# Kernel optimization log

Hardware: AMD Instinct MI355X
Metric: run time of the kernel (lower is better)

The kernel has to match this reference:

```python
import jax, jax.numpy as jnp
import numpy as np

E = 8          # number of tasks/experts (grown via new_task in the original)
B = 4096       # batch
CH, HT, WD = 3, 32, 32
D = CH * HT * WD   # 3072 flattened image dim
H = 1024       # hidden_dim
L = 512        # latent_dim
C = 100        # classes
TEMP = 2.0     # self.temperature


def setup_inputs() -> dict:
    key = jax.random.key(0)
    ks = jax.random.split(key, 32)
    def w(k, shape, fan_in):
        return jax.random.normal(k, shape, jnp.float32) * (1.0 / np.sqrt(fan_in))
    z = lambda shape: jnp.zeros(shape, jnp.float32)
    return {
        "x": jax.random.normal(ks[0], (B, CH, HT, WD), jnp.float32),
        # Gate autoencoder (per-expert stacked): encoder D->H->H->L, decoder L->H->H->D
        "enc_w0": w(ks[1], (E, D, H), D), "enc_b0": z((E, H)),
        "enc_w1": w(ks[2], (E, H, H), H), "enc_b1": z((E, H)),
        "enc_w2": w(ks[3], (E, H, L), H), "enc_b2": z((E, L)),
        "dec_w0": w(ks[4], (E, L, H), L), "dec_b0": z((E, H)),
        "dec_w1": w(ks[5], (E, H, H), H), "dec_b1": z((E, H)),
        "dec_w2": w(ks[6], (E, H, D), H), "dec_b2": z((E, D)),
        # Expert MLP (per-expert stacked): L->H->H->C
        "exp_w0": w(ks[7], (E, L, H), L), "exp_b0": z((E, H)),
        "exp_w1": w(ks[8], (E, H, H), H), "exp_b1": z((E, H)),
        "exp_w2": w(ks[9], (E, H, C), H), "exp_b2": z((E, C)),
    }


def reference(x, enc_w0, enc_b0, enc_w1, enc_b1, enc_w2, enc_b2,
              dec_w0, dec_b0, dec_w1, dec_b1, dec_w2, dec_b2,
              exp_w0, exp_b0, exp_w1, exp_b1, exp_w2, exp_b2):
    relu = jax.nn.relu
    b = x.shape[0]
    xf = x.reshape(b, -1)                                            # [B, D]
    # --- all gates in one batched pass (replaces python loop over gates) ---
    h = relu(jnp.einsum('bd,edh->ebh', xf, enc_w0) + enc_b0[:, None, :])
    h = relu(jnp.einsum('ebh,ehk->ebk', h, enc_w1) + enc_b1[:, None, :])
    lat = jnp.einsum('ebh,ehl->ebl', h, enc_w2) + enc_b2[:, None, :]  # [E, B, L]
    g = relu(jnp.einsum('ebl,elh->ebh', lat, dec_w0) + dec_b0[:, None, :])
    g = relu(jnp.einsum('ebh,ehk->ebk', g, dec_w1) + dec_b1[:, None, :])
    recon_flat = jnp.einsum('ebh,ehd->ebd', g, dec_w2) + dec_b2[:, None, :]  # [E, B, D]
    # L1 reconstruction error, mean over (C,H,W) == mean over flattened D
    err = jnp.mean(jnp.abs(recon_flat - xf[None]), axis=-1)          # [E, B]
    relevance_scores = jax.nn.softmax(-err / TEMP, axis=0)           # softmax over experts
    indices = jnp.argmin(err, axis=0)                                # [B]
    min_err = jnp.min(err, axis=0)                                   # [B]
    mask = jnp.arange(err.shape[0])[:, None] == indices[None, :]     # [E, B] bool
    # --- all experts densely, then select per-sample winner (same math as
    # the original masked gather/MLP/scatter: each row gets its argmin expert) ---
    e = relu(jnp.einsum('ebl,elh->ebh', lat, exp_w0) + exp_b0[:, None, :])
    e = relu(jnp.einsum('ebh,ehk->ebk', e, exp_w1) + exp_b1[:, None, :])
    exp_out = jnp.einsum('ebh,ehc->ebc', e, exp_w2) + exp_b2[:, None, :]  # [E, B, C]
    logits = jnp.take_along_axis(exp_out, indices[None, :, None], axis=0)[0]  # [B, C]
    reconstructions = recon_flat.reshape((err.shape[0],) + x.shape)  # [E, B, C, H, W]
    return (logits, reconstructions, indices, min_err, relevance_scores, mask)
```

## Files before the change

kernel.cpp:

```cpp
#include <hip/hip_runtime.h>
#include <hip/hip_fp16.h>

#define E_ 8
#define B_ 4096
#define D_ 3072
#define H_ 1024
#define L_ 512
#define C_ 100

#define RECON_OFF  409600ull
#define IDX_OFF    101072896ull
#define MINERR_OFF 101076992ull
#define REL_OFF    101081088ull
#define MASK_OFF   101113856ull

typedef _Float16 half8 __attribute__((ext_vector_type(8)));
typedef float floatx4 __attribute__((ext_vector_type(4)));

#define AS1 __attribute__((address_space(1)))
#define AS3 __attribute__((address_space(3)))

__device__ __forceinline__ void gl16(const void* g, void* l) {
  __builtin_amdgcn_global_load_lds((const AS1 unsigned int*)g, (AS3 unsigned int*)l, 16, 0, 0);
}

enum { OM_HILO = 0, OM_HI = 1, OM_F32 = 2, OM_RECON = 3 };

template <int OM, bool RELU, bool SPLIT>
__launch_bounds__(256, 2)
__global__ void gemm_k(const _Float16* __restrict__ Ah, const _Float16* __restrict__ Al,
                       const _Float16* __restrict__ Bh, const _Float16* __restrict__ Bl,
                       const float* __restrict__ bias, int biasN,
                       _Float16* __restrict__ Oh, _Float16* __restrict__ Ol,
                       float* __restrict__ Of, const float* __restrict__ Xf,
                       float* __restrict__ errOut,
                       int N, int K, int Npad, int Nstore, long aStrideE)
{
  const int M = B_;
  const int mBlocks = M >> 7;
  const int bx = blockIdx.x;
  const int mb = bx % mBlocks;
  const int nb = bx / mBlocks;
  const int e = blockIdx.y;
  const int m0 = mb << 7, n0 = nb << 7;
  const int tid = threadIdx.x;
  const int wave = tid >> 6, lane = tid & 63;
  const int wy = wave >> 1, wx = wave & 1;
  const int q = lane >> 4, t = lane & 15;

  __shared__ __align__(16) _Float16 sAh[128 * 32];
  __shared__ __align__(16) _Float16 sBh[128 * 32];
  __shared__ __align__(16) _Float16 sAl[SPLIT ? 128 * 32 : 8];
  __shared__ __align__(16) _Float16 sBl[SPLIT ? 128 * 32 : 8];
  __shared__ float ebuf[OM == OM_RECON ? 256 : 1];

  const size_t aoff = (size_t)(m0 + wave * 32 + (lane >> 2)) * K + (lane & 3) * 8;
  const size_t boff = (size_t)(n0 + wave * 32 + (lane >> 2)) * K + (lane & 3) * 8;
  const _Float16* pAh = Ah + (size_t)e * aStrideE + aoff;
  const _Float16* pBh = Bh + (size_t)e * Npad * K + boff;
  const _Float16* pAl = SPLIT ? (Al + (size_t)e * aStrideE + aoff) : (const _Float16*)nullptr;
  const _Float16* pBl = SPLIT ? (Bl + (size_t)e * Npad * K + boff) : (const _Float16*)nullptr;
  _Float16* dAh = &sAh[(wave * 32) * 32];
  _Float16* dBh = &sBh[(wave * 32) * 32];
  _Float16* dAl = &sAl[SPLIT ? (wave * 32) * 32 : 0];
  _Float16* dBl = &sBl[SPLIT ? (wave * 32) * 32 : 0];

  floatx4 acc[4][4] = {};
  floatx4 acx[4][4] = {};

  for (int kt = 0; kt < K; kt += 32) {
    __syncthreads();
    gl16(pAh, dAh);
    gl16(pAh + (size_t)16 * K, dAh + 16 * 32);
    gl16(pBh, dBh);
    gl16(pBh + (size_t)16 * K, dBh + 16 * 32);
    if (SPLIT) {
      gl16(pAl, dAl);
      gl16(pAl + (size_t)16 * K, dAl + 16 * 32);
      gl16(pBl, dBl);
      gl16(pBl + (size_t)16 * K, dBl + 16 * 32);
    }
    pAh += 32; pBh += 32;
    if (SPLIT) { pAl += 32; pBl += 32; }
    __syncthreads();

    half8 a_h[4], b_h[4], a_l[4], b_l[4];
#pragma unroll
    for (int i = 0; i < 4; ++i) {
      a_h[i] = *(const half8*)&sAh[(wy * 64 + i * 16 + t) * 32 + q * 8];
      b_h[i] = *(const half8*)&sBh[(wx * 64 + i * 16 + t) * 32 + q * 8];
      if (SPLIT) {
        a_l[i] = *(const half8*)&sAl[(wy * 64 + i * 16 + t) * 32 + q * 8];
        b_l[i] = *(const half8*)&sBl[(wx * 64 + i * 16 + t) * 32 + q * 8];
      }
    }
#pragma unroll
    for (int i = 0; i < 4; ++i)
#pragma unroll
      for (int j = 0; j < 4; ++j) {
        acc[i][j] = __builtin_amdgcn_mfma_f32_16x16x32_f16(a_h[i], b_h[j], acc[i][j], 0, 0, 0);
        if (SPLIT) {
          acx[i][j] = __builtin_amdgcn_mfma_f32_16x16x32_f16(a_h[i], b_l[j], acx[i][j], 0, 0, 0);
          acx[i][j] = __builtin_amdgcn_mfma_f32_16x16x32_f16(a_l[i], b_h[j], acx[i][j], 0, 0, 0);
        }
      }
  }

  float esum[4][4];
#pragma unroll
  for (int i = 0; i < 4; ++i)
#pragma unroll
    for (int r = 0; r < 4; ++r) esum[i][r] = 0.0f;

#pragma unroll
  for (int j = 0; j < 4; ++j) {
    const int gcol = n0 + wx * 64 + j * 16 + t;
    float bj = 0.0f;
    if (OM == OM_F32) { if (gcol < biasN) bj = bias[e * biasN + gcol]; }
    else bj = bias[e * biasN + gcol];
#pragma unroll
    for (int i = 0; i < 4; ++i)
#pragma unroll
      for (int r = 0; r < 4; ++r) {
        float v = acc[i][j][r];
        if (SPLIT) v += acx[i][j][r] * (1.0f / 4096.0f);
        v += bj;
        if (RELU) v = fmaxf(v, 0.0f);
        const int grow = m0 + wy * 64 + i * 16 + q * 4 + r;
        if (OM == OM_HILO) {
          const size_t o = (size_t)e * M * N + (size_t)grow * N + gcol;
          _Float16 h = (_Float16)v;
          Oh[o] = h;
          Ol[o] = (_Float16)((v - (float)h) * 4096.0f);
        } else if (OM == OM_HI) {
          Oh[(size_t)e * M * N + (size_t)grow * N + gcol] = (_Float16)v;
        } else if (OM == OM_F32) {
          if (gcol < Nstore)
            Of[(size_t)e * M * Nstore + (size_t)grow * Nstore + gcol] = v;
        } else {
          const size_t o = (size_t)e * M * N + (size_t)grow * N + gcol;
          Of[o] = v;
          esum[i][r] += fabsf(v - Xf[(size_t)grow * N + gcol]);
        }
      }
  }

  if (OM == OM_RECON) {
#pragma unroll
    for (int i = 0; i < 4; ++i)
#pragma unroll
      for (int r = 0; r < 4; ++r) {
        float s = esum[i][r];
        s += __shfl_xor(s, 1, 16);
        s += __shfl_xor(s, 2, 16);
        s += __shfl_xor(s, 4, 16);
        s += __shfl_xor(s, 8, 16);
        if (t == 0) ebuf[(wy * 64 + i * 16 + q * 4 + r) * 2 + wx] = s;
      }
    __syncthreads();
    if (tid < 128)
      atomicAdd(&errOut[(size_t)e * M + m0 + tid], ebuf[tid * 2] + ebuf[tid * 2 + 1]);
  }
}

__global__ void xsplit_k(const float* __restrict__ x, _Float16* __restrict__ xh,
                         _Float16* __restrict__ xl, int n)
{
  int i = blockIdx.x * 256 + threadIdx.x;
  if (i < n) {
    float v = x[i];
    _Float16 h = (_Float16)v;
    xh[i] = h;
    xl[i] = (_Float16)((v - (float)h) * 4096.0f);
  }
}

__global__ void wprep_k(const float* __restrict__ W, _Float16* __restrict__ Th,
                        _Float16* __restrict__ Tl, int K, int N, int Npad)
{
  __shared__ float tile[32][33];
  const int e = blockIdx.z;
  const int k0 = blockIdx.x * 32, n0 = blockIdx.y * 32;
  const int tx = threadIdx.x, ty = threadIdx.y;
  const float* We = W + (size_t)e * K * N;
#pragma unroll
  for (int s = 0; s < 4; ++s) {
    int k = k0 + ty + s * 8, n = n0 + tx;
    tile[ty + s * 8][tx] = (n < N) ? We[(size_t)k * N + n] : 0.0f;
  }
  __syncthreads();
#pragma unroll
  for (int s = 0; s < 4; ++s) {
    int n = n0 + ty + s * 8, k = k0 + tx;
    float v = tile[tx][ty + s * 8];
    size_t o = ((size_t)e * Npad + n) * K + k;
    _Float16 h = (_Float16)v;
    Th[o] = h;
    if (Tl) Tl[o] = (_Float16)((v - (float)h) * 4096.0f);
  }
}

__global__ void finalize_k(const float* __restrict__ err, float* __restrict__ out,
                           int* __restrict__ idxbuf)
{
  int b = blockIdx.x * 256 + threadIdx.x;
  if (b >= B_) return;
  float ev[E_];
  float mn = 3.4e38f;
  int am = 0;
#pragma unroll
  for (int e = 0; e < E_; ++e) {
    float v = err[(size_t)e * B_ + b] * (1.0f / 3072.0f);
    ev[e] = v;
    if (v < mn) { mn = v; am = e; }
  }
  float den = 0.0f, w[E_];
#pragma unroll
  for (int e = 0; e < E_; ++e) { w[e] = expf((mn - ev[e]) * 0.5f); den += w[e]; }
  float inv = 1.0f / den;
  out[IDX_OFF + b] = (float)am;
  out[MINERR_OFF + b] = mn;
#pragma unroll
  for (int e = 0; e < E_; ++e) {
    out[REL_OFF + (size_t)e * B_ + b] = w[e] * inv;
    out[MASK_OFF + (size_t)e * B_ + b] = (e == am) ? 1.0f : 0.0f;
  }
  idxbuf[b] = am;
}

__global__ void gather_k(const float* __restrict__ expout, const int* __restrict__ idx,
                         float* __restrict__ out)
{
  int b = blockIdx.x;
  int c = threadIdx.x;
  if (c < C_) out[(size_t)b * C_ + c] = expout[((size_t)idx[b] * B_ + b) * C_ + c];
}

extern "C" void kernel_launch(void* const* d_in, const int* in_sizes, int n_in,
                              void* d_out, int out_size, void* d_ws, size_t ws_size,
                              hipStream_t stream)
{
  const float* x      = (const float*)d_in[0];
  const float* enc_w0 = (const float*)d_in[1];
  const float* enc_b0 = (const float*)d_in[2];
  const float* enc_w1 = (const float*)d_in[3];
  const float* enc_b1 = (const float*)d_in[4];
  const float* enc_w2 = (const float*)d_in[5];
  const float* enc_b2 = (const float*)d_in[6];
  const float* dec_w0 = (const float*)d_in[7];
  const float* dec_b0 = (const float*)d_in[8];
  const float* dec_w1 = (const float*)d_in[9];
  const float* dec_b1 = (const float*)d_in[10];
  const float* dec_w2 = (const float*)d_in[11];
  const float* dec_b2 = (const float*)d_in[12];
  const float* exp_w0 = (const float*)d_in[13];
  const float* exp_b0 = (const float*)d_in[14];
  const float* exp_w1 = (const float*)d_in[15];
  const float* exp_b1 = (const float*)d_in[16];
  const float* exp_w2 = (const float*)d_in[17];
  const float* exp_b2 = (const float*)d_in[18];

  char* ws = (char*)d_ws;
  _Float16* xh     = (_Float16*)(ws + 0);
  _Float16* xl     = (_Float16*)(ws + 25165824);
  _Float16* WTh    = (_Float16*)(ws + 50331648);
  _Float16* WTl    = (_Float16*)(ws + 100663296);
  _Float16* lath   = (_Float16*)(ws + 150994944);
  _Float16* latl   = (_Float16*)(ws + 184549376);
  _Float16* g2h    = (_Float16*)(ws + 218103808);
  _Float16* g2l    = (_Float16*)(ws + 285212672);
  float*    expout = (float*)   (ws + 352321536);
  float*    errb   = (float*)   (ws + 365428736);
  int*      idxb   = (int*)     (ws + 365559808);

  float* out = (float*)d_out;
  float* recon = out + RECON_OFF;
  _Float16* bufAh = (_Float16*)recon;
  _Float16* bufAl = bufAh + (size_t)E_ * B_ * H_;
  _Float16* bufBh = bufAl + (size_t)E_ * B_ * H_;
  _Float16* bufBl = bufBh + (size_t)E_ * B_ * H_;

  hipMemsetAsync(errb, 0, (size_t)E_ * B_ * 4, stream);
  xsplit_k<<<(B_ * D_ + 255) / 256, 256, 0, stream>>>(x, xh, xl, B_ * D_);

  dim3 wb(32, 8);

  wprep_k<<<dim3(96, 32, E_), wb, 0, stream>>>(enc_w0, WTh, WTl, 3072, 1024, 1024);
  gemm_k<OM_HILO, true, true><<<dim3(32 * 8, E_), 256, 0, stream>>>(
      xh, xl, WTh, WTl, enc_b0, 1024, bufAh, bufAl, nullptr, nullptr, nullptr,
      1024, 3072, 1024, 1024, 0L);
  wprep_k<<<dim3(32, 32, E_), wb, 0, stream>>>(enc_w1, WTh, WTl, 1024, 1024, 1024);
  gemm_k<OM_HILO, true, true><<<dim3(32 * 8, E_), 256, 0, stream>>>(
      bufAh, bufAl, WTh, WTl, enc_b1, 1024, bufBh, bufBl, nullptr, nullptr, nullptr,
      1024, 1024, 1024, 1024, (long)B_ * H_);
  wprep_k<<<dim3(32, 16, E_), wb, 0, stream>>>(enc_w2, WTh, WTl, 1024, 512, 512);
  gemm_k<OM_HILO, false, true><<<dim3(32 * 4, E_), 256, 0, stream>>>(
      bufBh, bufBl, WTh, WTl, enc_b2, 512, lath, latl, nullptr, nullptr, nullptr,
      512, 1024, 512, 512, (long)B_ * H_);
  wprep_k<<<dim3(16, 32, E_), wb, 0, stream>>>(exp_w0, WTh, nullptr, 512, 1024, 1024);
  gemm_k<OM_HI, true, false><<<dim3(32 * 8, E_), 256, 0, stream>>>(
      lath, nullptr, WTh, nullptr, exp_b0, 1024, bufAh, nullptr, nullptr, nullptr, nullptr,
      1024, 512, 1024, 1024, (long)B_ * L_);
  wprep_k<<<dim3(32, 32, E_), wb, 0, stream>>>(exp_w1, WTh, nullptr, 1024, 1024, 1024);
  gemm_k<OM_HI, true, false><<<dim3(32 * 8, E_), 256, 0, stream>>>(
      bufAh, nullptr, WTh, nullptr, exp_b1, 1024, bufBh, nullptr, nullptr, nullptr, nullptr,
      1024, 1024, 1024, 1024, (long)B_ * H_);
  wprep_k<<<dim3(32, 4, E_), wb, 0, stream>>>(exp_w2, WTh, nullptr, 1024, 100, 128);
  gemm_k<OM_F32, false, false><<<dim3(32 * 1, E_), 256, 0, stream>>>(
      bufBh, nullptr, WTh, nullptr, exp_b2, 100, nullptr, nullptr, expout, nullptr, nullptr,
      128, 1024, 128, 100, (long)B_ * H_);
  wprep_k<<<dim3(16, 32, E_), wb, 0, stream>>>(dec_w0, WTh, WTl, 512, 1024, 1024);
  gemm_k<OM_HILO, true, true><<<dim3(32 * 8, E_), 256, 0, stream>>>(
      lath, latl, WTh, WTl, dec_b0, 1024, bufAh, bufAl, nullptr, nullptr, nullptr,
      1024, 512, 1024, 1024, (long)B_ * L_);
  wprep_k<<<dim3(32, 32, E_), wb, 0, stream>>>(dec_w1, WTh, WTl, 1024, 1024, 1024);
  gemm_k<OM_HILO, true, true><<<dim3(32 * 8, E_), 256, 0, stream>>>(
      bufAh, bufAl, WTh, WTl, dec_b1, 1024, g2h, g2l, nullptr, nullptr, nullptr,
      1024, 1024, 1024, 1024, (long)B_ * H_);
  wprep_k<<<dim3(32, 96, E_), wb, 0, stream>>>(dec_w2, WTh, WTl, 1024, 3072, 3072);
  gemm_k<OM_RECON, false, true><<<dim3(32 * 24, E_), 256, 0, stream>>>(
      g2h, g2l, WTh, WTl, dec_b2, 3072, nullptr, nullptr, recon, x, errb,
      3072, 1024, 3072, 3072, (long)B_ * H_);

  finalize_k<<<(B_ + 255) / 256, 256, 0, stream>>>(errb, out, idxb);
  gather_k<<<B_, 128, 0, stream>>>(expout, idxb, out);
}
```

Measured before the change: 2.969 ms.

## Merge split-precision accumulators, swizzle LDS layout, raise occupancy bounds

Removes the scaling of low-part fp16 residuals so the cross-term MFMAs accumulate into the main accumulator, eliminating a second 4x4 accumulator array and cutting register pressure. Launch bounds are raised so more blocks can reside per CU. An XOR swizzle is applied to the LDS tile columns at load and read time to reduce bank conflicts. Unscaled residuals risk fp16 subnormal precision loss in the split-precision products.

```diff
diff --git a/kernel.cpp b/kernel.cpp
--- a/kernel.cpp
+++ b/kernel.cpp
@@ -27,7 +27,7 @@
 enum { OM_HILO = 0, OM_HI = 1, OM_F32 = 2, OM_RECON = 3 };
 
 template <int OM, bool RELU, bool SPLIT>
-__launch_bounds__(256, 2)
+__launch_bounds__(256, SPLIT ? 3 : 4)
 __global__ void gemm_k(const _Float16* __restrict__ Ah, const _Float16* __restrict__ Al,
                        const _Float16* __restrict__ Bh, const _Float16* __restrict__ Bl,
                        const float* __restrict__ bias, int biasN,
@@ -54,8 +54,9 @@
   __shared__ __align__(16) _Float16 sBl[SPLIT ? 128 * 32 : 8];
   __shared__ float ebuf[OM == OM_RECON ? 256 : 1];
 
-  const size_t aoff = (size_t)(m0 + wave * 32 + (lane >> 2)) * K + (lane & 3) * 8;
-  const size_t boff = (size_t)(n0 + wave * 32 + (lane >> 2)) * K + (lane & 3) * 8;
+  const int swzc = ((lane & 3) ^ ((lane >> 3) & 3)) * 8;
+  const size_t aoff = (size_t)(m0 + wave * 32 + (lane >> 2)) * K + swzc;
+  const size_t boff = (size_t)(n0 + wave * 32 + (lane >> 2)) * K + swzc;
   const _Float16* pAh = Ah + (size_t)e * aStrideE + aoff;
   const _Float16* pBh = Bh + (size_t)e * Npad * K + boff;
   const _Float16* pAl = SPLIT ? (Al + (size_t)e * aStrideE + aoff) : (const _Float16*)nullptr;
@@ -65,8 +66,9 @@
   _Float16* dAl = &sAl[SPLIT ? (wave * 32) * 32 : 0];
   _Float16* dBl = &sBl[SPLIT ? (wave * 32) * 32 : 0];
 
+  const int rcol = (q ^ ((t >> 1) & 3)) * 8;
+
   floatx4 acc[4][4] = {};
-  floatx4 acx[4][4] = {};
 
   for (int kt = 0; kt < K; kt += 32) {
     __syncthreads();
@@ -87,11 +89,11 @@
     half8 a_h[4], b_h[4], a_l[4], b_l[4];
 #pragma unroll
     for (int i = 0; i < 4; ++i) {
-      a_h[i] = *(const half8*)&sAh[(wy * 64 + i * 16 + t) * 32 + q * 8];
-      b_h[i] = *(const half8*)&sBh[(wx * 64 + i * 16 + t) * 32 + q * 8];
+      a_h[i] = *(const half8*)&sAh[(wy * 64 + i * 16 + t) * 32 + rcol];
+      b_h[i] = *(const half8*)&sBh[(wx * 64 + i * 16 + t) * 32 + rcol];
       if (SPLIT) {
-        a_l[i] = *(const half8*)&sAl[(wy * 64 + i * 16 + t) * 32 + q * 8];
-        b_l[i] = *(const half8*)&sBl[(wx * 64 + i * 16 + t) * 32 + q * 8];
+        a_l[i] = *(const half8*)&sAl[(wy * 64 + i * 16 + t) * 32 + rcol];
+        b_l[i] = *(const half8*)&sBl[(wx * 64 + i * 16 + t) * 32 + rcol];
       }
     }
 #pragma unroll
@@ -100,8 +102,8 @@
       for (int j = 0; j < 4; ++j) {
         acc[i][j] = __builtin_amdgcn_mfma_f32_16x16x32_f16(a_h[i], b_h[j], acc[i][j], 0, 0, 0);
         if (SPLIT) {
-          acx[i][j] = __builtin_amdgcn_mfma_f32_16x16x32_f16(a_h[i], b_l[j], acx[i][j], 0, 0, 0);
-          acx[i][j] = __builtin_amdgcn_mfma_f32_16x16x32_f16(a_l[i], b_h[j], acx[i][j], 0, 0, 0);
+          acc[i][j] = __builtin_amdgcn_mfma_f32_16x16x32_f16(a_h[i], b_l[j], acc[i][j], 0, 0, 0);
+          acc[i][j] = __builtin_amdgcn_mfma_f32_16x16x32_f16(a_l[i], b_h[j], acc[i][j], 0, 0, 0);
         }
       }
   }
@@ -122,16 +124,14 @@
     for (int i = 0; i < 4; ++i)
 #pragma unroll
       for (int r = 0; r < 4; ++r) {
-        float v = acc[i][j][r];
-        if (SPLIT) v += acx[i][j][r] * (1.0f / 4096.0f);
-        v += bj;
+        float v = acc[i][j][r] + bj;
         if (RELU) v = fmaxf(v, 0.0f);
         const int grow = m0 + wy * 64 + i * 16 + q * 4 + r;
         if (OM == OM_HILO) {
           const size_t o = (size_t)e * M * N + (size_t)grow * N + gcol;
           _Float16 h = (_Float16)v;
           Oh[o] = h;
-          Ol[o] = (_Float16)((v - (float)h) * 4096.0f);
+          Ol[o] = (_Float16)(v - (float)h);
         } else if (OM == OM_HI) {
           Oh[(size_t)e * M * N + (size_t)grow * N + gcol] = (_Float16)v;
         } else if (OM == OM_F32) {
@@ -171,7 +171,7 @@
     float v = x[i];
     _Float16 h = (_Float16)v;
     xh[i] = h;
-    xl[i] = (_Float16)((v - (float)h) * 4096.0f);
+    xl[i] = (_Float16)(v - (float)h);
   }
 }
 
@@ -196,7 +196,7 @@
     size_t o = ((size_t)e * Npad + n) * K + k;
     _Float16 h = (_Float16)v;
     Th[o] = h;
-    if (Tl) Tl[o] = (_Float16)((v - (float)h) * 4096.0f);
+    if (Tl) Tl[o] = (_Float16)(v - (float)h);
   }
 }
 
```

Result: faster. 2.806 ms (-5.5%).
